# Kernel optimization log

Hardware: AMD Instinct MI355X
Metric: run time of the kernel (lower is better)

Reference implementation:

```python
import jax, jax.numpy as jnp
import numpy as np

B, N, DIM = 4, 2048, 1024
HEADS, DIM_HEAD = 16, 64
INNER = HEADS * DIM_HEAD


def setup_inputs() -> dict:
    key = jax.random.key(0)
    kx, kw = jax.random.split(key)
    x = jax.random.normal(kx, (B, N, DIM), dtype=jnp.float32)
    # Dense kernel [in_features, out_features], no bias
    w_qkv = jax.random.normal(kw, (DIM, 3 * INNER), dtype=jnp.float32) * (DIM ** -0.5)
    return {"x": x, "w_qkv": w_qkv}


def reference(x, w_qkv):
    scale = DIM_HEAD ** (-0.5)
    qkv = jnp.einsum('bnc,cf->bnf', x, w_qkv)  # [B, N, 3*INNER]
    q, k, v = jnp.split(qkv, 3, axis=-1)
    # 'b n (h d) -> b h n d'
    def to_heads(t):
        return t.reshape(B, N, HEADS, DIM_HEAD).transpose(0, 2, 1, 3)
    q, k, v = map(to_heads, (q, k, v))
    dots = jnp.einsum('bhid,bhjd->bhij', q, k) * scale  # [B, H, N, N]
    attn = jax.nn.softmax(dots, axis=-1)
    out = jnp.einsum('bhij,bhjd->bhid', attn, v)  # [B, H, N, D]
    # 'b h n d -> b n (h d)'
    return out.transpose(0, 2, 1, 3).reshape(B, N, INNER)
```

## Files before the change

### kernel.cpp

```cpp
#include <hip/hip_runtime.h>
#include <hip/hip_bf16.h>
#include <math.h>

typedef __bf16 bf16x2 __attribute__((ext_vector_type(2)));
typedef __bf16 bf16x4 __attribute__((ext_vector_type(4)));
typedef __bf16 bf16x8 __attribute__((ext_vector_type(8)));
typedef float f32x4 __attribute__((ext_vector_type(4)));
typedef float f32x16 __attribute__((ext_vector_type(16)));

#define MFMA16(a, b, c) __builtin_amdgcn_mfma_f32_16x16x32_bf16(a, b, c, 0, 0, 0)
#define MFMA32(a, b, c) __builtin_amdgcn_mfma_f32_32x32x16_bf16(a, b, c, 0, 0, 0)
#define QSCALE 0.1803368801111204f

__device__ __forceinline__ void gload_lds16(const __bf16* g, __bf16* l) {
  __builtin_amdgcn_global_load_lds((const __attribute__((address_space(1))) void*)g,
                                   (__attribute__((address_space(3))) void*)l,
                                   16, 0, 0);
}

__global__ __launch_bounds__(256) void convert_x(const float* __restrict__ in,
                                                 __bf16* __restrict__ out) {
  int i = blockIdx.x * 256 + threadIdx.x;
  float4 v = ((const float4*)in)[i];
  bf16x4 o = {(__bf16)v.x, (__bf16)v.y, (__bf16)v.z, (__bf16)v.w};
  *(bf16x4*)&out[i * 4] = o;
}

__global__ __launch_bounds__(256) void transpose_w(const float* __restrict__ W,
                                                   __bf16* __restrict__ Wt) {
  __shared__ __bf16 tile[64][65];
  const int bx = blockIdx.x;
  const int by = blockIdx.y;
  const int t = threadIdx.x;
  const int lr = t >> 6;
  const int lc = t & 63;
  const float sc = (bx < 16) ? QSCALE : 1.0f;
#pragma unroll
  for (int i = 0; i < 16; ++i) {
    int r = lr + i * 4;
    tile[r][lc] = (__bf16)(W[(size_t)(by * 64 + r) * 3072 + bx * 64 + lc] * sc);
  }
  __syncthreads();
#pragma unroll
  for (int i = 0; i < 16; ++i) {
    int r = lr + i * 4;
    Wt[(size_t)(bx * 64 + r) * 1024 + by * 64 + lc] = tile[lc][r];
  }
}

__global__ __launch_bounds__(256) void gemm_qkv(const __bf16* __restrict__ X,
                                                const __bf16* __restrict__ Wt,
                                                __bf16* __restrict__ QK,
                                                __bf16* __restrict__ Vt) {
  __shared__ __bf16 As[128 * 32];
  __shared__ __bf16 Bs[128 * 32];
  const int t = threadIdx.x;
  const int lane = t & 63;
  const int wave = t >> 6;
  const int quad = lane >> 4;
  const int l16 = lane & 15;
  const int n0 = blockIdx.x * 128;
  const int m0 = blockIdx.y * 128;
  const int wm = (wave & 1) * 64;
  const int wn = (wave >> 1) * 64;

  const __bf16* Ag = &X[(size_t)(m0 + wave * 16 + (lane >> 2)) * 1024 + (lane & 3) * 8];
  const __bf16* Bg = &Wt[(size_t)(n0 + wave * 16 + (lane >> 2)) * 1024 + (lane & 3) * 8];
  __bf16* As0 = &As[wave * 512];
  __bf16* As1 = &As[2048 + wave * 512];
  __bf16* Bs0 = &Bs[wave * 512];
  __bf16* Bs1 = &Bs[2048 + wave * 512];

  f32x4 acc[4][4] = {};

  for (int k0 = 0; k0 < 1024; k0 += 32) {
    gload_lds16(Ag + k0, As0);
    gload_lds16(Ag + (size_t)64 * 1024 + k0, As1);
    gload_lds16(Bg + k0, Bs0);
    gload_lds16(Bg + (size_t)64 * 1024 + k0, Bs1);
    __syncthreads();

    bf16x8 af[4], bf[4];
#pragma unroll
    for (int mi = 0; mi < 4; ++mi)
      af[mi] = *(const bf16x8*)&As[(wm + mi * 16 + l16) * 32 + quad * 8];
#pragma unroll
    for (int ni = 0; ni < 4; ++ni)
      bf[ni] = *(const bf16x8*)&Bs[(wn + ni * 16 + l16) * 32 + quad * 8];
#pragma unroll
    for (int mi = 0; mi < 4; ++mi)
#pragma unroll
      for (int ni = 0; ni < 4; ++ni)
        acc[mi][ni] = MFMA16(af[mi], bf[ni], acc[mi][ni]);
    __syncthreads();
  }

  if (n0 < 2048) {
#pragma unroll
    for (int mi = 0; mi < 4; ++mi)
#pragma unroll
      for (int ni = 0; ni < 4; ++ni)
#pragma unroll
        for (int r = 0; r < 4; ++r) {
          int row = m0 + wm + mi * 16 + quad * 4 + r;
          int col = n0 + wn + ni * 16 + l16;
          QK[(size_t)row * 2048 + col] = (__bf16)acc[mi][ni][r];
        }
  } else {
#pragma unroll
    for (int mi = 0; mi < 4; ++mi)
#pragma unroll
      for (int ni = 0; ni < 4; ++ni) {
        int v = n0 + wn + ni * 16 + l16 - 2048;
        int hh = v >> 6, d = v & 63;
        int row0 = m0 + wm + mi * 16 + quad * 4;
        int bb = row0 >> 11, key = row0 & 2047;
        bf16x4 pk = {(__bf16)acc[mi][ni][0], (__bf16)acc[mi][ni][1],
                     (__bf16)acc[mi][ni][2], (__bf16)acc[mi][ni][3]};
        *(bf16x4*)&Vt[((size_t)(bb * 16 + hh) * 64 + d) * 2048 + key] = pk;
      }
  }
}

#define AT_LD 72

__global__ __launch_bounds__(256) void attn(const __bf16* __restrict__ QK,
                                            const __bf16* __restrict__ Vt,
                                            float* __restrict__ Out) {
  const int h = blockIdx.y;
  const int b = blockIdx.z;
  const int t = threadIdx.x;
  const int lane = t & 63;
  const int wave = t >> 6;
  const int l31 = lane & 31;
  const int half = lane >> 5;
  const int q0w = blockIdx.x * 128 + wave * 32;

  const size_t base = (size_t)b * 2048 * 2048;
  const __bf16* Qb = QK + base + h * 64;
  const __bf16* Kb = QK + base + 1024 + h * 64;
  const __bf16* Vtb = Vt + (size_t)(b * 16 + h) * 64 * 2048;

  __shared__ __bf16 Ks[64 * AT_LD];
  __shared__ __bf16 Vs[64 * AT_LD];

  bf16x8 qf[4];
#pragma unroll
  for (int dc = 0; dc < 4; ++dc)
    qf[dc] = *(const bf16x8*)&Qb[(size_t)(q0w + l31) * 2048 + dc * 16 + half * 8];

  f32x16 o[2] = {};
  float lsum = 0.0f;

  const int srow = t >> 2;
  const int sc = (t & 3) * 16;
  const int prow = (srow & 51) | ((srow & 4) << 1) | ((srow & 8) >> 1);

  for (int kv0 = 0; kv0 < 2048; kv0 += 64) {
    bf16x8 k0v = *(const bf16x8*)&Kb[(size_t)(kv0 + srow) * 2048 + sc];
    bf16x8 k1v = *(const bf16x8*)&Kb[(size_t)(kv0 + srow) * 2048 + sc + 8];
    bf16x8 v0v = *(const bf16x8*)&Vtb[(size_t)srow * 2048 + kv0 + sc];
    bf16x8 v1v = *(const bf16x8*)&Vtb[(size_t)srow * 2048 + kv0 + sc + 8];
    __syncthreads();
    *(bf16x8*)&Ks[prow * AT_LD + sc] = k0v;
    *(bf16x8*)&Ks[prow * AT_LD + sc + 8] = k1v;
    *(bf16x8*)&Vs[srow * AT_LD + sc] = v0v;
    *(bf16x8*)&Vs[srow * AT_LD + sc + 8] = v1v;
    __syncthreads();

    bf16x8 pf[4];
#pragma unroll
    for (int kt = 0; kt < 2; ++kt) {
      f32x16 c = {};
#pragma unroll
      for (int dc = 0; dc < 4; ++dc) {
        bf16x8 kf = *(const bf16x8*)&Ks[(kt * 32 + l31) * AT_LD + dc * 16 + half * 8];
        c = MFMA32(kf, qf[dc], c);
      }
#pragma unroll
      for (int kkl = 0; kkl < 2; ++kkl) {
        bf16x8 f;
#pragma unroll
        for (int j = 0; j < 8; ++j) {
          float e = __builtin_amdgcn_exp2f(c[8 * kkl + 4 * (j >> 2) + (j & 3)]);
          lsum += e;
          f[j] = (__bf16)e;
        }
        pf[kt * 2 + kkl] = f;
      }
    }

#pragma unroll
    for (int dt = 0; dt < 2; ++dt)
#pragma unroll
      for (int kk = 0; kk < 4; ++kk) {
        bf16x8 vf = *(const bf16x8*)&Vs[(dt * 32 + l31) * AT_LD + kk * 16 + half * 8];
        o[dt] = MFMA32(pf[kk], vf, o[dt]);
      }
  }

  lsum += __shfl_xor(lsum, 32);
  float inv = 1.0f / lsum;

  float iv[16];
#pragma unroll
  for (int r = 0; r < 16; ++r)
    iv[r] = __shfl(inv, (r & 3) + 8 * (r >> 2) + 4 * half);

#pragma unroll
  for (int dt = 0; dt < 2; ++dt)
#pragma unroll
    for (int r = 0; r < 16; ++r) {
      int qr = (r & 3) + 8 * (r >> 2) + 4 * half;
      Out[(size_t)(b * 2048 + q0w + qr) * 1024 + h * 64 + dt * 32 + l31] =
          o[dt][r] * iv[r];
    }
}

extern "C" void kernel_launch(void* const* d_in, const int* in_sizes, int n_in,
                              void* d_out, int out_size, void* d_ws, size_t ws_size,
                              hipStream_t stream) {
  const float* x = (const float*)d_in[0];
  const float* w = (const float*)d_in[1];
  float* out = (float*)d_out;

  __bf16* Wt = (__bf16*)d_ws;
  __bf16* QK = Wt + (size_t)3072 * 1024;
  __bf16* Xb = QK + (size_t)8192 * 2048;
  __bf16* Vtr = Xb + (size_t)8192 * 1024;

  convert_x<<<8192, 256, 0, stream>>>(x, Xb);
  transpose_w<<<dim3(48, 16), 256, 0, stream>>>(w, Wt);
  gemm_qkv<<<dim3(24, 64), 256, 0, stream>>>(Xb, Wt, QK, Vtr);
  attn<<<dim3(16, 16, 4), 256, 0, stream>>>(QK, Vtr, out);
}
```

Before: 246.7 us.

## Double-buffer K/V tiles in attention with register prefetch two tiles ahead

Switches the attention kernel's K/V shared-memory staging to two LDS buffers. Global loads for tile it+2 are issued into registers while tile it+1 is written to LDS and tile it is computed, and the two barriers per iteration drop to one. Row-sum accumulation is split across four partial sums to shorten the dependent add chain. This doubles LDS use per block and adds register pressure for the in-flight prefetch, which could lower occupancy.

```diff
diff --git a/kernel.cpp b/kernel.cpp
--- a/kernel.cpp
+++ b/kernel.cpp
@@ -141,8 +141,8 @@
   const __bf16* Kb = QK + base + 1024 + h * 64;
   const __bf16* Vtb = Vt + (size_t)(b * 16 + h) * 64 * 2048;
 
-  __shared__ __bf16 Ks[64 * AT_LD];
-  __shared__ __bf16 Vs[64 * AT_LD];
+  __shared__ __bf16 Ks[2][64 * AT_LD];
+  __shared__ __bf16 Vs[2][64 * AT_LD];
 
   bf16x8 qf[4];
 #pragma unroll
@@ -150,23 +150,50 @@
     qf[dc] = *(const bf16x8*)&Qb[(size_t)(q0w + l31) * 2048 + dc * 16 + half * 8];
 
   f32x16 o[2] = {};
-  float lsum = 0.0f;
+  f32x4 ls = {0.0f, 0.0f, 0.0f, 0.0f};
 
   const int srow = t >> 2;
   const int sc = (t & 3) * 16;
   const int prow = (srow & 51) | ((srow & 4) << 1) | ((srow & 8) >> 1);
 
-  for (int kv0 = 0; kv0 < 2048; kv0 += 64) {
-    bf16x8 k0v = *(const bf16x8*)&Kb[(size_t)(kv0 + srow) * 2048 + sc];
-    bf16x8 k1v = *(const bf16x8*)&Kb[(size_t)(kv0 + srow) * 2048 + sc + 8];
-    bf16x8 v0v = *(const bf16x8*)&Vtb[(size_t)srow * 2048 + kv0 + sc];
-    bf16x8 v1v = *(const bf16x8*)&Vtb[(size_t)srow * 2048 + kv0 + sc + 8];
-    __syncthreads();
-    *(bf16x8*)&Ks[prow * AT_LD + sc] = k0v;
-    *(bf16x8*)&Ks[prow * AT_LD + sc + 8] = k1v;
-    *(bf16x8*)&Vs[srow * AT_LD + sc] = v0v;
-    *(bf16x8*)&Vs[srow * AT_LD + sc + 8] = v1v;
-    __syncthreads();
+  const __bf16* Kst = &Kb[(size_t)srow * 2048 + sc];
+  const __bf16* Vst = &Vtb[(size_t)srow * 2048 + sc];
+
+  bf16x8 k0v = *(const bf16x8*)&Kst[0];
+  bf16x8 k1v = *(const bf16x8*)&Kst[8];
+  bf16x8 v0v = *(const bf16x8*)&Vst[0];
+  bf16x8 v1v = *(const bf16x8*)&Vst[8];
+  *(bf16x8*)&Ks[0][prow * AT_LD + sc] = k0v;
+  *(bf16x8*)&Ks[0][prow * AT_LD + sc + 8] = k1v;
+  *(bf16x8*)&Vs[0][srow * AT_LD + sc] = v0v;
+  *(bf16x8*)&Vs[0][srow * AT_LD + sc + 8] = v1v;
+  k0v = *(const bf16x8*)&Kst[(size_t)64 * 2048];
+  k1v = *(const bf16x8*)&Kst[(size_t)64 * 2048 + 8];
+  v0v = *(const bf16x8*)&Vst[64];
+  v1v = *(const bf16x8*)&Vst[64 + 8];
+  __syncthreads();
+
+  for (int it = 0; it < 32; ++it) {
+    const int cur = it & 1;
+    __bf16* Kw = &Ks[cur ^ 1][0];
+    __bf16* Vw = &Vs[cur ^ 1][0];
+    const __bf16* Kr = &Ks[cur][0];
+    const __bf16* Vr = &Vs[cur][0];
+
+    if (it < 31) {
+      *(bf16x8*)&Kw[prow * AT_LD + sc] = k0v;
+      *(bf16x8*)&Kw[prow * AT_LD + sc + 8] = k1v;
+      *(bf16x8*)&Vw[srow * AT_LD + sc] = v0v;
+      *(bf16x8*)&Vw[srow * AT_LD + sc + 8] = v1v;
+    }
+    if (it < 30) {
+      size_t ko = (size_t)(it + 2) * 64 * 2048;
+      int vo = (it + 2) * 64;
+      k0v = *(const bf16x8*)&Kst[ko];
+      k1v = *(const bf16x8*)&Kst[ko + 8];
+      v0v = *(const bf16x8*)&Vst[vo];
+      v1v = *(const bf16x8*)&Vst[vo + 8];
+    }
 
     bf16x8 pf[4];
 #pragma unroll
@@ -174,7 +201,7 @@
       f32x16 c = {};
 #pragma unroll
       for (int dc = 0; dc < 4; ++dc) {
-        bf16x8 kf = *(const bf16x8*)&Ks[(kt * 32 + l31) * AT_LD + dc * 16 + half * 8];
+        bf16x8 kf = *(const bf16x8*)&Kr[(kt * 32 + l31) * AT_LD + dc * 16 + half * 8];
         c = MFMA32(kf, qf[dc], c);
       }
 #pragma unroll
@@ -183,7 +210,7 @@
 #pragma unroll
         for (int j = 0; j < 8; ++j) {
           float e = __builtin_amdgcn_exp2f(c[8 * kkl + 4 * (j >> 2) + (j & 3)]);
-          lsum += e;
+          ls[j & 3] += e;
           f[j] = (__bf16)e;
         }
         pf[kt * 2 + kkl] = f;
@@ -194,11 +221,14 @@
     for (int dt = 0; dt < 2; ++dt)
 #pragma unroll
       for (int kk = 0; kk < 4; ++kk) {
-        bf16x8 vf = *(const bf16x8*)&Vs[(dt * 32 + l31) * AT_LD + kk * 16 + half * 8];
+        bf16x8 vf = *(const bf16x8*)&Vr[(dt * 32 + l31) * AT_LD + kk * 16 + half * 8];
         o[dt] = MFMA32(pf[kk], vf, o[dt]);
       }
-  }
-
+
+    __syncthreads();
+  }
+
+  float lsum = (ls[0] + ls[1]) + (ls[2] + ls[3]);
   lsum += __shfl_xor(lsum, 32);
   float inv = 1.0f / lsum;
 
```

Result: no change. 247.4 us (+0.3%).

## Widen attention KV tile to 128 and interleave PV MFMAs per subtile with priority hints

Applied to the files above, without the earlier changes.

The attention loop now stages 128 keys per iteration instead of 64, halving the number of barrier pairs, and loads wider per-thread chunks. Each 32-key subtile's PV MFMAs are issued right after its softmax exponentials rather than after all QK tiles, and s_setprio raises wave priority around the MFMA bursts to help overlap exp work with matrix work across waves. The single row-sum accumulator is split into four partial sums to shorten the dependency chain. LDS use grows, which may affect occupancy.

```diff
diff --git a/kernel.cpp b/kernel.cpp
--- a/kernel.cpp
+++ b/kernel.cpp
@@ -123,6 +123,7 @@
 }
 
 #define AT_LD 72
+#define VT_LD 136
 
 __global__ __launch_bounds__(256) void attn(const __bf16* __restrict__ QK,
                                             const __bf16* __restrict__ Vt,
@@ -141,8 +142,8 @@
   const __bf16* Kb = QK + base + 1024 + h * 64;
   const __bf16* Vtb = Vt + (size_t)(b * 16 + h) * 64 * 2048;
 
-  __shared__ __bf16 Ks[64 * AT_LD];
-  __shared__ __bf16 Vs[64 * AT_LD];
+  __shared__ __bf16 Ks[128 * AT_LD];
+  __shared__ __bf16 Vs[64 * VT_LD];
 
   bf16x8 qf[4];
 #pragma unroll
@@ -150,55 +151,69 @@
     qf[dc] = *(const bf16x8*)&Qb[(size_t)(q0w + l31) * 2048 + dc * 16 + half * 8];
 
   f32x16 o[2] = {};
-  float lsum = 0.0f;
-
-  const int srow = t >> 2;
-  const int sc = (t & 3) * 16;
-  const int prow = (srow & 51) | ((srow & 4) << 1) | ((srow & 8) >> 1);
-
-  for (int kv0 = 0; kv0 < 2048; kv0 += 64) {
-    bf16x8 k0v = *(const bf16x8*)&Kb[(size_t)(kv0 + srow) * 2048 + sc];
-    bf16x8 k1v = *(const bf16x8*)&Kb[(size_t)(kv0 + srow) * 2048 + sc + 8];
-    bf16x8 v0v = *(const bf16x8*)&Vtb[(size_t)srow * 2048 + kv0 + sc];
-    bf16x8 v1v = *(const bf16x8*)&Vtb[(size_t)srow * 2048 + kv0 + sc + 8];
-    __syncthreads();
-    *(bf16x8*)&Ks[prow * AT_LD + sc] = k0v;
-    *(bf16x8*)&Ks[prow * AT_LD + sc + 8] = k1v;
-    *(bf16x8*)&Vs[srow * AT_LD + sc] = v0v;
-    *(bf16x8*)&Vs[srow * AT_LD + sc + 8] = v1v;
-    __syncthreads();
-
-    bf16x8 pf[4];
-#pragma unroll
-    for (int kt = 0; kt < 2; ++kt) {
+  f32x4 ls = {0.0f, 0.0f, 0.0f, 0.0f};
+
+  const int srow = t >> 1;
+  const int scK = (t & 1) * 32;
+  const int prow = (srow & ~12) | ((srow & 4) << 1) | ((srow & 8) >> 1);
+  const int vrow = t >> 2;
+  const int scV = (t & 3) * 32;
+
+  for (int kv0 = 0; kv0 < 2048; kv0 += 128) {
+    bf16x8 ka[4], va[4];
+#pragma unroll
+    for (int i = 0; i < 4; ++i)
+      ka[i] = *(const bf16x8*)&Kb[(size_t)(kv0 + srow) * 2048 + scK + i * 8];
+#pragma unroll
+    for (int i = 0; i < 4; ++i)
+      va[i] = *(const bf16x8*)&Vtb[(size_t)vrow * 2048 + kv0 + scV + i * 8];
+    __syncthreads();
+#pragma unroll
+    for (int i = 0; i < 4; ++i)
+      *(bf16x8*)&Ks[prow * AT_LD + scK + i * 8] = ka[i];
+#pragma unroll
+    for (int i = 0; i < 4; ++i)
+      *(bf16x8*)&Vs[vrow * VT_LD + scV + i * 8] = va[i];
+    __syncthreads();
+
+#pragma unroll
+    for (int ktt = 0; ktt < 4; ++ktt) {
       f32x16 c = {};
+      __builtin_amdgcn_s_setprio(1);
 #pragma unroll
       for (int dc = 0; dc < 4; ++dc) {
-        bf16x8 kf = *(const bf16x8*)&Ks[(kt * 32 + l31) * AT_LD + dc * 16 + half * 8];
+        bf16x8 kf = *(const bf16x8*)&Ks[(ktt * 32 + l31) * AT_LD + dc * 16 + half * 8];
         c = MFMA32(kf, qf[dc], c);
       }
+      __builtin_amdgcn_s_setprio(0);
+
+      bf16x8 pf[2];
 #pragma unroll
       for (int kkl = 0; kkl < 2; ++kkl) {
         bf16x8 f;
 #pragma unroll
         for (int j = 0; j < 8; ++j) {
           float e = __builtin_amdgcn_exp2f(c[8 * kkl + 4 * (j >> 2) + (j & 3)]);
-          lsum += e;
+          ls[j & 3] += e;
           f[j] = (__bf16)e;
         }
-        pf[kt * 2 + kkl] = f;
+        pf[kkl] = f;
       }
+
+      __builtin_amdgcn_s_setprio(1);
+#pragma unroll
+      for (int dt = 0; dt < 2; ++dt)
+#pragma unroll
+        for (int kkl = 0; kkl < 2; ++kkl) {
+          bf16x8 vf = *(const bf16x8*)&Vs[(dt * 32 + l31) * VT_LD +
+                                          (ktt * 2 + kkl) * 16 + half * 8];
+          o[dt] = MFMA32(pf[kkl], vf, o[dt]);
+        }
+      __builtin_amdgcn_s_setprio(0);
     }
-
-#pragma unroll
-    for (int dt = 0; dt < 2; ++dt)
-#pragma unroll
-      for (int kk = 0; kk < 4; ++kk) {
-        bf16x8 vf = *(const bf16x8*)&Vs[(dt * 32 + l31) * AT_LD + kk * 16 + half * 8];
-        o[dt] = MFMA32(pf[kk], vf, o[dt]);
-      }
-  }
-
+  }
+
+  float lsum = (ls[0] + ls[1]) + (ls[2] + ls[3]);
   lsum += __shfl_xor(lsum, 32);
   float inv = 1.0f / lsum;
 
```

Measured after the change: 245.9 us. Within noise of the previous version (-0.3%).

## Load K and V fragments directly from global memory, dropping LDS staging

Applied to the files above, without the earlier changes.

The attention kernel no longer stages K and V tiles through shared memory with two block barriers per iteration. Each wave now reads its MFMA operand fragments straight from global memory and relies on L1/L2 caches for reuse across the four waves. The row-sum accumulator is also split into four independent partial sums to shorten the dependency chain. The risk is more global/cache traffic and exposed load latency with no software prefetch, since each K/V element is now fetched by every wave.

```diff
diff --git a/kernel.cpp b/kernel.cpp
--- a/kernel.cpp
+++ b/kernel.cpp
@@ -122,8 +122,6 @@
   }
 }
 
-#define AT_LD 72
-
 __global__ __launch_bounds__(256) void attn(const __bf16* __restrict__ QK,
                                             const __bf16* __restrict__ Vt,
                                             float* __restrict__ Out) {
@@ -141,40 +139,28 @@
   const __bf16* Kb = QK + base + 1024 + h * 64;
   const __bf16* Vtb = Vt + (size_t)(b * 16 + h) * 64 * 2048;
 
-  __shared__ __bf16 Ks[64 * AT_LD];
-  __shared__ __bf16 Vs[64 * AT_LD];
-
   bf16x8 qf[4];
 #pragma unroll
   for (int dc = 0; dc < 4; ++dc)
     qf[dc] = *(const bf16x8*)&Qb[(size_t)(q0w + l31) * 2048 + dc * 16 + half * 8];
 
   f32x16 o[2] = {};
-  float lsum = 0.0f;
-
-  const int srow = t >> 2;
-  const int sc = (t & 3) * 16;
-  const int prow = (srow & 51) | ((srow & 4) << 1) | ((srow & 8) >> 1);
+  f32x4 ls = {0.0f, 0.0f, 0.0f, 0.0f};
+
+  const int krow = (l31 & ~12) | ((l31 & 4) << 1) | ((l31 & 8) >> 1);
+
+  const __bf16* Kl = &Kb[(size_t)krow * 2048];
+  const __bf16* Vl = &Vtb[(size_t)l31 * 2048];
 
   for (int kv0 = 0; kv0 < 2048; kv0 += 64) {
-    bf16x8 k0v = *(const bf16x8*)&Kb[(size_t)(kv0 + srow) * 2048 + sc];
-    bf16x8 k1v = *(const bf16x8*)&Kb[(size_t)(kv0 + srow) * 2048 + sc + 8];
-    bf16x8 v0v = *(const bf16x8*)&Vtb[(size_t)srow * 2048 + kv0 + sc];
-    bf16x8 v1v = *(const bf16x8*)&Vtb[(size_t)srow * 2048 + kv0 + sc + 8];
-    __syncthreads();
-    *(bf16x8*)&Ks[prow * AT_LD + sc] = k0v;
-    *(bf16x8*)&Ks[prow * AT_LD + sc + 8] = k1v;
-    *(bf16x8*)&Vs[srow * AT_LD + sc] = v0v;
-    *(bf16x8*)&Vs[srow * AT_LD + sc + 8] = v1v;
-    __syncthreads();
-
     bf16x8 pf[4];
 #pragma unroll
     for (int kt = 0; kt < 2; ++kt) {
       f32x16 c = {};
 #pragma unroll
       for (int dc = 0; dc < 4; ++dc) {
-        bf16x8 kf = *(const bf16x8*)&Ks[(kt * 32 + l31) * AT_LD + dc * 16 + half * 8];
+        bf16x8 kf = *(const bf16x8*)&Kl[(size_t)(kv0 + kt * 32) * 2048 +
+                                        dc * 16 + half * 8];
         c = MFMA32(kf, qf[dc], c);
       }
 #pragma unroll
@@ -183,7 +169,7 @@
 #pragma unroll
         for (int j = 0; j < 8; ++j) {
           float e = __builtin_amdgcn_exp2f(c[8 * kkl + 4 * (j >> 2) + (j & 3)]);
-          lsum += e;
+          ls[j & 3] += e;
           f[j] = (__bf16)e;
         }
         pf[kt * 2 + kkl] = f;
@@ -194,11 +180,13 @@
     for (int dt = 0; dt < 2; ++dt)
 #pragma unroll
       for (int kk = 0; kk < 4; ++kk) {
-        bf16x8 vf = *(const bf16x8*)&Vs[(dt * 32 + l31) * AT_LD + kk * 16 + half * 8];
+        bf16x8 vf = *(const bf16x8*)&Vl[(size_t)dt * 32 * 2048 + kv0 +
+                                        kk * 16 + half * 8];
         o[dt] = MFMA32(pf[kk], vf, o[dt]);
       }
   }
 
+  float lsum = (ls[0] + ls[1]) + (ls[2] + ls[3]);
   lsum += __shfl_xor(lsum, 32);
   float inv = 1.0f / lsum;
 
```

Result: slower. 437.1 us (+77.2%).
